# Kernel optimization log

Measured on AMD Instinct MI355X. Metric: run time of the kernel, lower is better.

## Reference

```python
import jax, jax.numpy as jnp
import numpy as np

BIG_CONST = 1000000.0
LN_EPS = 1e-5

B, S, D = 2, 1024, 1024
N, H = 16, D // 16            # n_head, d_head
POS_LEN = 2 * S - 1


def setup_inputs() -> dict:
    key = jax.random.key(0)
    ks = jax.random.split(key, 16)
    std_qkv = np.sqrt(1.0 / float(D + N * H))   # EinsumLayer init: 1/sqrt(fan_in+fan_out)
    std_post = np.sqrt(1.0 / float(N * H + D))
    return {
        "q": jax.random.normal(ks[0], (B, S, D), jnp.float32),
        "k": jax.random.normal(ks[1], (B, S, D), jnp.float32),
        "v": jax.random.normal(ks[2], (B, S, D), jnp.float32),
        "pos_enc": jax.random.normal(ks[3], (POS_LEN, D), jnp.float32),
        "attn_mask": jax.random.randint(ks[4], (B, 1, 1, S), 0, 2, jnp.int32),
        "q_w": jax.random.normal(ks[5], (D, N, H), jnp.float32) * std_qkv,
        "k_w": jax.random.normal(ks[6], (D, N, H), jnp.float32) * std_qkv,
        "k_b": jnp.zeros((N, H), jnp.float32),
        "v_w": jax.random.normal(ks[7], (D, N, H), jnp.float32) * std_qkv,
        "v_b": jnp.zeros((N, H), jnp.float32),
        "r_w_bias": jax.random.uniform(ks[8], (N, 1, H), jnp.float32, 0.0, 0.1),
        "r_r_bias": jax.random.uniform(ks[9], (N, 1, H), jnp.float32, 0.0, 0.1),
        "r_kernel": jax.random.uniform(ks[10], (N, D, H), jnp.float32, 0.0, 0.1),
        "post_w": jax.random.normal(ks[11], (N, H, D), jnp.float32) * std_post,
        "post_b": jnp.zeros((D,), jnp.float32),
        "ln_g": jnp.ones((D,), jnp.float32),
        "ln_b": jnp.zeros((D,), jnp.float32),
    }


def reference(q, k, v, pos_enc, attn_mask, q_w, k_w, k_b, v_w, v_b,
              r_w_bias, r_r_bias, r_kernel, post_w, post_b, ln_g, ln_b):
    input_q = q
    d_head = q_w.shape[-1]
    normalizer = 1.0 / np.sqrt(d_head)

    # head projections -> [B, N, L, H]
    qh = jnp.einsum('bld,dnh->bnlh', q, q_w)
    kh = jnp.einsum('bld,dnh->bnlh', k, k_w) + k_b[None, :, None, :] * 0 + jnp.transpose(k_b, (0, 1))[None, :, None, :] * 0 + k_b.reshape(1, k_b.shape[0], 1, k_b.shape[1])
    kh = jnp.einsum('bld,dnh->bnlh', k, k_w) + k_b.reshape(1, -1, 1, d_head)
    vh = jnp.einsum('bld,dnh->bnlh', v, v_w) + v_b.reshape(1, -1, 1, d_head)

    # content score: (q + r_w_bias) @ k^T * normalizer   [B,N,S,S]
    content = jnp.einsum('bnqh,bnkh->bnqk', qh + r_w_bias[None], kh) * normalizer

    # positional term (rel_shift with shift=0): r = pos_enc @ r_kernel -> [N, P, H]
    r = jnp.einsum('pd,ndh->nph', pos_enc, r_kernel)
    pos_scores = jnp.einsum('bnqh,nph->bnqp', qh + r_r_bias[None], r) * normalizer
    # shift=0 => reshape-swap + narrow + reshape-back is an exact identity; then narrow to k_len
    k_len = kh.shape[-2]
    pos_term = pos_scores[..., :k_len]

    attn_score = (content + pos_term).astype(jnp.float32)
    attn_score = attn_score - BIG_CONST * attn_mask.astype(jnp.float32)
    attn_dist = jax.nn.softmax(attn_score, axis=-1)

    out = jnp.einsum('bnqk,bnkh->bnqh', attn_dist, vh)          # [B,N,S,H]
    attn_out = jnp.einsum('bnlh,nhd->bld', out, post_w) + post_b

    x = input_q + attn_out
    mu = jnp.mean(x, axis=-1, keepdims=True)
    var = jnp.mean(jnp.square(x - mu), axis=-1, keepdims=True)
    return (x - mu) / jnp.sqrt(var + LN_EPS) * ln_g + ln_b
```

## Files before the change

### kernel.cpp

```cpp
#include <hip/hip_runtime.h>
#include <cstddef>
#include <cstdint>

typedef unsigned short u16;
typedef unsigned int   u32;

#define S_LEN  1024
#define NHEAD  16
#define HDIM   64
#define DMODEL 1024
#define NORMSC 0.125f
#define BIGC   1000000.0f
#define LOG2E  1.44269504088896f
#define SC2    (0.125f * 1.44269504088896f)

typedef __bf16 bf16x8 __attribute__((ext_vector_type(8)));
typedef float  f32x4  __attribute__((ext_vector_type(4)));

#define MFMA16(a, b, c) __builtin_amdgcn_mfma_f32_16x16x32_bf16((a), (b), (c), 0, 0, 0)

__device__ __forceinline__ u16 f2bf(float f) {
    u32 u = __float_as_uint(f);
    u32 r = (u + 0x7fffu + ((u >> 16) & 1u)) >> 16;
    return (u16)r;
}
__device__ __forceinline__ float bf2f(u32 v) {
    return __uint_as_float(v << 16);
}
__device__ __forceinline__ float4 unp4(uint2 u) {
    float4 f;
    f.x = bf2f(u.x & 0xffffu); f.y = bf2f(u.x >> 16);
    f.z = bf2f(u.y & 0xffffu); f.w = bf2f(u.y >> 16);
    return f;
}
__device__ __forceinline__ void async16(const void* g, void* l) {
    __builtin_amdgcn_global_load_lds(
        (__attribute__((address_space(1))) void*)(g),
        (__attribute__((address_space(3))) void*)(l), 16, 0, 0);
}

__global__ __launch_bounds__(256) void prep_all(
    const float* q, const float* k, const float* v, const float* pos,
    const float* qw, const float* kw, const float* vw, const float* pw, const float* rk,
    u16* qbf, u16* kbf, u16* vbf, u16* posb,
    u16* qwT, u16* kwT, u16* vwT, u16* pwT, u16* WrT)
{
    __shared__ float tb[32][33];
    const int bid = blockIdx.x, tid = threadIdx.x;
    if (bid < 7168) {
        const float* s; u16* d; int base;
        if (bid < 2048)      { s = q;   d = qbf;  base = bid; }
        else if (bid < 4096) { s = k;   d = kbf;  base = bid - 2048; }
        else if (bid < 6144) { s = v;   d = vbf;  base = bid - 4096; }
        else                 { s = pos; d = posb; base = bid - 6144; }
        const int i = base * 1024 + tid * 4;
        const float4 val = *(const float4*)&s[i];
        uint2 o;
        o.x = (u32)f2bf(val.x) | ((u32)f2bf(val.y) << 16);
        o.y = (u32)f2bf(val.z) | ((u32)f2bf(val.w) << 16);
        *(uint2*)&d[i] = o;
        return;
    }
    const int t = bid - 7168;
    const float* in; u16* out; int ild, r0, c0;
    if (t < 4096) {
        const int ts = t & 1023;
        if (t < 1024)      { in = qw; out = qwT; }
        else if (t < 2048) { in = kw; out = kwT; }
        else if (t < 3072) { in = vw; out = vwT; }
        else               { in = pw; out = pwT; }
        ild = 1024;
        r0 = (ts >> 5) * 32; c0 = (ts & 31) * 32;
    } else {
        const int ts = t - 4096;
        const int n = ts >> 6, tt = ts & 63;
        in = rk + (size_t)n * 65536; out = WrT + (size_t)n * 65536;
        ild = 64;
        r0 = (tt >> 1) * 32; c0 = (tt & 1) * 32;
    }
    const int tx = tid & 31, ty = tid >> 5;
    for (int i = ty; i < 32; i += 8)
        tb[i][tx] = in[(size_t)(r0 + i) * ild + c0 + tx];
    __syncthreads();
    for (int i = ty; i < 32; i += 8)
        out[(size_t)(c0 + i) * 1024 + r0 + tx] = f2bf(tb[tx][i]);
}

struct GJ { const u16* A; const u16* Bt; u16* C; int M; int k0; int klen; };

__global__ __launch_bounds__(256) void gemm_p(
    GJ j0, GJ j1, GJ j2, GJ j3, GJ j4, GJ j5, GJ j6, GJ j7, int nj)
{
    const int bid = blockIdx.x;
    const int c8 = bid & 7;
    const int x = (bid >> 3) & 7;
    int z, y;
    if (nj == 8) { z = c8; y = bid >> 6; }
    else         { z = c8 >> 1; y = ((c8 & 1) << 3) + (bid >> 6); }
    GJ g;
    switch (z) {
        case 0: g = j0; break; case 1: g = j1; break;
        case 2: g = j2; break; case 3: g = j3; break;
        case 4: g = j4; break; case 5: g = j5; break;
        case 6: g = j6; break; default: g = j7;
    }
    const int bm = y * 128;
    if (bm >= g.M) return;
    const int bn = x * 128;
    __shared__ u16 As[2][4096];
    __shared__ u16 Bs[2][4096];
    const int tid = threadIdx.x;
    const int w = tid >> 6, lane = tid & 63;
    const int wm = (w >> 1) * 64, wn = (w & 1) * 64;
    const int l15 = lane & 15, l16 = lane >> 4;
    f32x4 acc[4][4] = {};
    const char* Ab = (const char*)g.A;
    const char* Bb = (const char*)g.Bt;
    const int kend = g.k0 + g.klen;
    const int m0 = w * 1024 + lane * 16;
    const int m1 = (4 + w) * 1024 + lane * 16;
    const int r0w = m0 >> 6, rc0 = ((((m0 >> 4) & 3) + r0w) & 3) << 4;
    const int r1w = m1 >> 6, rc1 = ((((m1 >> 4) & 3) + r1w) & 3) << 4;
    async16(Ab + ((size_t)(bm + r0w) * 1024 + g.k0) * 2 + rc0, (char*)As[0] + m0);
    async16(Bb + ((size_t)(bn + r0w) * 1024 + g.k0) * 2 + rc0, (char*)Bs[0] + m0);
    async16(Ab + ((size_t)(bm + r1w) * 1024 + g.k0) * 2 + rc1, (char*)As[0] + m1);
    async16(Bb + ((size_t)(bn + r1w) * 1024 + g.k0) * 2 + rc1, (char*)Bs[0] + m1);
    const int rotA = ((l16 - l15) & 3) << 3;
    int buf = 0;
    for (int k0 = g.k0; k0 < kend; k0 += 32) {
        __syncthreads();
        const int kn = k0 + 32;
        if (kn < kend) {
            async16(Ab + ((size_t)(bm + r0w) * 1024 + kn) * 2 + rc0, (char*)As[buf ^ 1] + m0);
            async16(Bb + ((size_t)(bn + r0w) * 1024 + kn) * 2 + rc0, (char*)Bs[buf ^ 1] + m0);
            async16(Ab + ((size_t)(bm + r1w) * 1024 + kn) * 2 + rc1, (char*)As[buf ^ 1] + m1);
            async16(Bb + ((size_t)(bn + r1w) * 1024 + kn) * 2 + rc1, (char*)Bs[buf ^ 1] + m1);
        }
        bf16x8 af[4], bfr[4];
#pragma unroll
        for (int i = 0; i < 4; ++i)
            af[i] = *(const bf16x8*)&As[buf][(wm + i * 16 + l15) * 32 + rotA];
#pragma unroll
        for (int j = 0; j < 4; ++j)
            bfr[j] = *(const bf16x8*)&Bs[buf][(wn + j * 16 + l15) * 32 + rotA];
#pragma unroll
        for (int i = 0; i < 4; ++i)
#pragma unroll
            for (int j = 0; j < 4; ++j)
                acc[i][j] = MFMA16(af[i], bfr[j], acc[i][j]);
        buf ^= 1;
    }
#pragma unroll
    for (int i = 0; i < 4; ++i)
#pragma unroll
        for (int j = 0; j < 4; ++j) {
            const int c = bn + wn + j * 16 + l15;
#pragma unroll
            for (int rg = 0; rg < 4; ++rg) {
                const int m = bm + wm + i * 16 + l16 * 4 + rg;
                g.C[(size_t)m * 1024 + c] = f2bf(acc[i][j][rg]);
            }
        }
}

__global__ __launch_bounds__(256) void prep2(
    const u16* pk0, const u16* pk1, const u16* pr0, const u16* pr1,
    const u16* pv0, const u16* pv1, const u16* pq0, const u16* pq1,
    const float* kbi, const float* vbi, const float* rwb, const float* rrb,
    const int* mask, u16* keff, float* cc, u16* vT, u16* qhb)
{
    __shared__ float tb[32][33];
    const int bid = blockIdx.x, tid = threadIdx.x;
    if (bid < 2048) {
        const int t = bid * 256 + tid;
        const int row = t >> 4, li = t & 15;
        const int n = (row >> 10) & 15, kk = row & 1023, b = row >> 14;
        const size_t mi = ((size_t)(b * 1024 + kk)) * 1024 + n * 64 + li * 4;
        const size_t pi = ((size_t)kk) * 1024 + n * 64 + li * 4;
        const float4 k0v = unp4(*(const uint2*)&pk0[mi]);
        const float4 k1v = unp4(*(const uint2*)&pk1[mi]);
        const float4 r0v = unp4(*(const uint2*)&pr0[pi]);
        const float4 r1v = unp4(*(const uint2*)&pr1[pi]);
        const float4 kb4 = *(const float4*)&kbi[n * 64 + li * 4];
        float4 kv, rv;
        kv.x = k0v.x + k1v.x + kb4.x; kv.y = k0v.y + k1v.y + kb4.y;
        kv.z = k0v.z + k1v.z + kb4.z; kv.w = k0v.w + k1v.w + kb4.w;
        rv.x = r0v.x + r1v.x; rv.y = r0v.y + r1v.y;
        rv.z = r0v.z + r1v.z; rv.w = r0v.w + r1v.w;
        const float4 w1 = *(const float4*)&rwb[n * 64 + li * 4];
        const float4 w2 = *(const float4*)&rrb[n * 64 + li * 4];
        float s = w1.x * kv.x + w1.y * kv.y + w1.z * kv.z + w1.w * kv.w
                + w2.x * rv.x + w2.y * rv.y + w2.z * rv.z + w2.w * rv.w;
        uint2 o;
        o.x = (u32)f2bf(kv.x + rv.x) | ((u32)f2bf(kv.y + rv.y) << 16);
        o.y = (u32)f2bf(kv.z + rv.z) | ((u32)f2bf(kv.w + rv.w) << 16);
        *(uint2*)&keff[(size_t)row * 64 + li * 4] = o;
#pragma unroll
        for (int m = 1; m < 16; m <<= 1) s += __shfl_xor(s, m);
        if (li == 0)
            cc[row] = LOG2E * (NORMSC * s - BIGC * (float)mask[b * 1024 + kk]);
        return;
    }
    if (bid < 4096) {
        const int t = bid - 2048;
        const int head = t >> 6, tt = t & 63;
        const int b = head >> 4, n = head & 15;
        const int r0 = (tt >> 1) * 32, c0 = (tt & 1) * 32;
        const int tx = tid & 31, ty = tid >> 5;
        const float vb = vbi[n * 64 + c0 + tx];
        for (int i = ty; i < 32; i += 8) {
            const size_t idx = ((size_t)(b * 1024 + r0 + i)) * 1024 + n * 64 + c0 + tx;
            tb[i][tx] = bf2f(pv0[idx]) + bf2f(pv1[idx]) + vb;
        }
        __syncthreads();
        u16* out = vT + (size_t)head * 65536;
        for (int i = ty; i < 32; i += 8)
            out[(size_t)(c0 + i) * 1024 + r0 + tx] = f2bf(tb[tx][i]);
        return;
    }
    const int t = bid - 4096;
    const int e = t * 1024 + tid * 4;
    const int m = e >> 10, c = e & 1023;
    const float4 a = unp4(*(const uint2*)&pq0[e]);
    const float4 b4 = unp4(*(const uint2*)&pq1[e]);
    uint2 o;
    o.x = (u32)f2bf(a.x + b4.x) | ((u32)f2bf(a.y + b4.y) << 16);
    o.y = (u32)f2bf(a.z + b4.z) | ((u32)f2bf(a.w + b4.w) << 16);
    const int b2 = m >> 10, l = m & 1023, n = c >> 6, h = c & 63;
    *(uint2*)&qhb[(((size_t)(b2 * NHEAD + n)) * 1024 + l) * 64 + h] = o;
}

__global__ __launch_bounds__(128) void attn_mfma(
    const u16* qb, const u16* kb, const u16* vtb, const float* ccomb, u16* O)
{
    __shared__ u16   Ks[2][4096];
    __shared__ u16   Vs[2][4096];
    __shared__ __bf16 Ps[2][1024];
    const int tid = threadIdx.x;
    const int w = tid >> 6, lane = tid & 63;
    const int l15 = lane & 15, l16 = lane >> 4;
    const int bid = blockIdx.x;
    const int i128 = bid >> 3;
    const int head = (bid & 7) * 4 + (i128 >> 5);
    const int q0 = (i128 & 31) * 32;
    const int b = head >> 4, n = head & 15;
    const size_t hoff = (size_t)head * 65536;
    const u16* qh = qb + hoff;
    const char* khc = (const char*)(kb + hoff);
    const char* vtc = (const char*)(vtb + hoff);
    const float* cc = ccomb + head * 1024;
    __bf16* Pw = Ps[w];

    bf16x8 qf[2];
    {
        const size_t rb = ((size_t)(q0 + w * 16 + l15)) * 64 + l16 * 8;
        qf[0] = *(const bf16x8*)&qh[rb];
        qf[1] = *(const bf16x8*)&qh[rb + 32];
    }
    f32x4 Oacc[4] = {};
    float lsum[4] = {};

    const int sr0 = w * 32 + (lane >> 3);
    const int sc0 = lane & 7;
#pragma unroll
    for (int i = 0; i < 4; ++i) {
        const int r = sr0 + i * 8;
        async16(khc + r * 128 + (((sc0 + r) & 7) << 4), (char*)Ks[0] + r * 128 + sc0 * 16);
        async16(vtc + (size_t)r * 2048 + (((sc0 + r) & 7) << 4), (char*)Vs[0] + r * 128 + sc0 * 16);
    }
    int buf = 0;
    for (int kc = 0; kc < 16; ++kc) {
        __syncthreads();
        if (kc < 15) {
            const int kn = kc + 1;
#pragma unroll
            for (int i = 0; i < 4; ++i) {
                const int r = sr0 + i * 8;
                async16(khc + kn * 8192 + r * 128 + (((sc0 + r) & 7) << 4),
                        (char*)Ks[buf ^ 1] + r * 128 + sc0 * 16);
                async16(vtc + (size_t)r * 2048 + kn * 128 + (((sc0 + r) & 7) << 4),
                        (char*)Vs[buf ^ 1] + r * 128 + sc0 * 16);
            }
        }
        const u16* Kb = Ks[buf];
        const u16* Vb = Vs[buf];
        f32x4 sc[4];
#pragma unroll
        for (int j = 0; j < 4; ++j) {
            const int rk2 = j * 16 + l15;
            const int base = rk2 * 64;
            f32x4 a = {0.f, 0.f, 0.f, 0.f};
            a = MFMA16(qf[0], *(const bf16x8*)&Kb[base + (((l16 - rk2) & 7) << 3)], a);
            a = MFMA16(qf[1], *(const bf16x8*)&Kb[base + (((l16 + 4 - rk2) & 7) << 3)], a);
            const float cadd = cc[kc * 64 + j * 16 + l15];
            sc[j] = a * SC2 + cadd;
        }
#pragma unroll
        for (int j = 0; j < 4; ++j) {
            const int cg = j * 2 + (l15 >> 3);
#pragma unroll
            for (int rg = 0; rg < 4; ++rg) {
                const float p = exp2f(sc[j][rg]);
                lsum[rg] += p;
                const int row = l16 * 4 + rg;
                Pw[row * 64 + (((cg - row) & 7) << 3) + (l15 & 7)] = (__bf16)p;
            }
        }
        bf16x8 pf[2];
#pragma unroll
        for (int f = 0; f < 2; ++f)
            pf[f] = *(const bf16x8*)&Pw[l15 * 64 + (((f * 4 + l16 - l15) & 7) << 3)];
#pragma unroll
        for (int t4 = 0; t4 < 4; ++t4) {
#pragma unroll
            for (int f = 0; f < 2; ++f) {
                const int vr = t4 * 16 + l15;
                const int ch = f * 4 + l16;
                const bf16x8 vf = *(const bf16x8*)&Vb[vr * 64 + (((ch - vr) & 7) << 3)];
                Oacc[t4] = MFMA16(pf[f], vf, Oacc[t4]);
            }
        }
        buf ^= 1;
    }
    float inv[4];
#pragma unroll
    for (int rg = 0; rg < 4; ++rg) {
        float s = lsum[rg];
#pragma unroll
        for (int m = 1; m < 16; m <<= 1) s += __shfl_xor(s, m);
        inv[rg] = 1.0f / s;
    }
#pragma unroll
    for (int t4 = 0; t4 < 4; ++t4) {
#pragma unroll
        for (int rg = 0; rg < 4; ++rg) {
            const int srow = q0 + w * 16 + l16 * 4 + rg;
            const int col = n * 64 + t4 * 16 + l15;
            O[((size_t)b * 1024 + srow) * 1024 + col] = f2bf(Oacc[t4][rg] * inv[rg]);
        }
    }
}

__global__ __launch_bounds__(256) void ln_kernel(
    const u16* __restrict__ p0, const u16* __restrict__ p1,
    const u16* __restrict__ p2, const u16* __restrict__ p3,
    const float* __restrict__ resid, const float* __restrict__ pb,
    const float* __restrict__ g, const float* __restrict__ bb,
    float* __restrict__ out)
{
    const int row = blockIdx.x;
    const int tid = threadIdx.x;
    const size_t i = (size_t)row * DMODEL + tid * 4;
    const float4 a0 = unp4(*(const uint2*)&p0[i]);
    const float4 a1 = unp4(*(const uint2*)&p1[i]);
    const float4 a2 = unp4(*(const uint2*)&p2[i]);
    const float4 a3 = unp4(*(const uint2*)&p3[i]);
    const float4 rr = *(const float4*)&resid[i];
    const float4 pv = *(const float4*)&pb[tid * 4];
    float4 v;
    v.x = a0.x + a1.x + a2.x + a3.x + rr.x + pv.x;
    v.y = a0.y + a1.y + a2.y + a3.y + rr.y + pv.y;
    v.z = a0.z + a1.z + a2.z + a3.z + rr.z + pv.z;
    v.w = a0.w + a1.w + a2.w + a3.w + rr.w + pv.w;
    float s1 = v.x + v.y + v.z + v.w;
    float s2 = v.x * v.x + v.y * v.y + v.z * v.z + v.w * v.w;
#pragma unroll
    for (int off = 32; off; off >>= 1) {
        s1 += __shfl_down(s1, off);
        s2 += __shfl_down(s2, off);
    }
    __shared__ float rb[8];
    if ((tid & 63) == 0) { rb[tid >> 6] = s1; rb[4 + (tid >> 6)] = s2; }
    __syncthreads();
    if (tid == 0) {
        rb[0] = rb[0] + rb[1] + rb[2] + rb[3];
        rb[4] = rb[4] + rb[5] + rb[6] + rb[7];
    }
    __syncthreads();
    s1 = rb[0]; s2 = rb[4];
    const float mu = s1 * (1.0f / DMODEL);
    const float var = s2 * (1.0f / DMODEL) - mu * mu;
    const float rstd = rsqrtf(var + 1e-5f);
    const float4 gv = *(const float4*)&g[tid * 4];
    const float4 bv = *(const float4*)&bb[tid * 4];
    float4 o;
    o.x = (v.x - mu) * rstd * gv.x + bv.x;
    o.y = (v.y - mu) * rstd * gv.y + bv.y;
    o.z = (v.z - mu) * rstd * gv.z + bv.z;
    o.w = (v.w - mu) * rstd * gv.w + bv.w;
    *(float4*)&out[i] = o;
}

extern "C" void kernel_launch(void* const* d_in, const int* in_sizes, int n_in,
                              void* d_out, int out_size, void* d_ws, size_t ws_size,
                              hipStream_t stream)
{
    (void)in_sizes; (void)n_in; (void)out_size; (void)ws_size;
    const float* q   = (const float*)d_in[0];
    const float* k   = (const float*)d_in[1];
    const float* v   = (const float*)d_in[2];
    const float* pos = (const float*)d_in[3];
    const int*   msk = (const int*)d_in[4];
    const float* qw  = (const float*)d_in[5];
    const float* kw  = (const float*)d_in[6];
    const float* kbi = (const float*)d_in[7];
    const float* vw  = (const float*)d_in[8];
    const float* vbi = (const float*)d_in[9];
    const float* rwb = (const float*)d_in[10];
    const float* rrb = (const float*)d_in[11];
    const float* rk  = (const float*)d_in[12];
    const float* pw  = (const float*)d_in[13];
    const float* pb  = (const float*)d_in[14];
    const float* lg  = (const float*)d_in[15];
    const float* lb  = (const float*)d_in[16];
    float* out = (float*)d_out;

    float* fb = (float*)d_ws;
    float* cc   = fb;
    u16* us   = (u16*)(cc + 32768);
    u16* qbf  = us;
    u16* kbf  = qbf + 2097152;
    u16* vbf  = kbf + 2097152;
    u16* posb = vbf + 2097152;
    u16* qwT  = posb + 1048576;
    u16* kwT  = qwT + 1048576;
    u16* vwT  = kwT + 1048576;
    u16* pwT  = vwT + 1048576;
    u16* WrT  = pwT + 1048576;
    u16* qhb  = WrT + 1048576;
    u16* keffb= qhb + 2097152;
    u16* vTb  = keffb + 2097152;
    u16* pq0  = vTb + 2097152;
    u16* pq1  = pq0 + 2097152;
    u16* pk0  = pq1 + 2097152;
    u16* pk1  = pk0 + 2097152;
    u16* pv0  = pk1 + 2097152;
    u16* pv1  = pv0 + 2097152;
    u16* pr0  = pv1 + 2097152;
    u16* pr1  = pr0 + 1048576;
    u16* po0  = pr1 + 1048576;
    u16* po1  = po0 + 2097152;
    u16* po2  = po1 + 2097152;
    u16* po3  = po2 + 2097152;
    u16* Obf  = qbf;

    dim3 blk(256);
    prep_all<<<12288, blk, 0, stream>>>(q, k, v, pos, qw, kw, vw, pw, rk,
                                        qbf, kbf, vbf, posb, qwT, kwT, vwT, pwT, WrT);

    GJ jq0 = {qbf,  qwT, pq0, 2048, 0,   512};
    GJ jq1 = {qbf,  qwT, pq1, 2048, 512, 512};
    GJ jk0 = {kbf,  kwT, pk0, 2048, 0,   512};
    GJ jk1 = {kbf,  kwT, pk1, 2048, 512, 512};
    GJ jv0 = {vbf,  vwT, pv0, 2048, 0,   512};
    GJ jv1 = {vbf,  vwT, pv1, 2048, 512, 512};
    GJ jp0 = {posb, WrT, pr0, 1024, 0,   512};
    GJ jp1 = {posb, WrT, pr1, 1024, 512, 512};
    gemm_p<<<1024, blk, 0, stream>>>(jq0, jq1, jk0, jk1, jv0, jv1, jp0, jp1, 8);

    prep2<<<6144, blk, 0, stream>>>(pk0, pk1, pr0, pr1, pv0, pv1, pq0, pq1,
                                    kbi, vbi, rwb, rrb, msk, keffb, cc, vTb, qhb);

    attn_mfma<<<1024, dim3(128), 0, stream>>>(qhb, keffb, vTb, cc, Obf);

    GJ jo0 = {Obf, pwT, po0, 2048, 0,   256};
    GJ jo1 = {Obf, pwT, po1, 2048, 256, 256};
    GJ jo2 = {Obf, pwT, po2, 2048, 512, 256};
    GJ jo3 = {Obf, pwT, po3, 2048, 768, 256};
    gemm_p<<<512, blk, 0, stream>>>(jo0, jo1, jo2, jo3, jo0, jo0, jo0, jo0, 4);

    ln_kernel<<<2048, blk, 0, stream>>>(po0, po1, po2, po3, q, pb, lg, lb, out);
}
```

Before: 203.3 us.

## Load GEMM MFMA fragments directly from global memory, dropping LDS staging

The batched projection GEMM kernel no longer stages A and B tiles through double-buffered shared memory with async copies. Each wave now loads its MFMA fragments straight from global memory into registers, prefetching the next k-step while issuing MFMAs on the current one. This removes LDS traffic and the per-step __syncthreads. In exchange, the two waves sharing a tile row or column each fetch the same data from global memory (relying on cache), and each load reads only 16 bytes per row with a strided pattern.

```diff
diff --git a/kernel.cpp b/kernel.cpp
--- a/kernel.cpp
+++ b/kernel.cpp
@@ -107,49 +107,51 @@
     const int bm = y * 128;
     if (bm >= g.M) return;
     const int bn = x * 128;
-    __shared__ u16 As[2][4096];
-    __shared__ u16 Bs[2][4096];
     const int tid = threadIdx.x;
     const int w = tid >> 6, lane = tid & 63;
     const int wm = (w >> 1) * 64, wn = (w & 1) * 64;
     const int l15 = lane & 15, l16 = lane >> 4;
     f32x4 acc[4][4] = {};
-    const char* Ab = (const char*)g.A;
-    const char* Bb = (const char*)g.Bt;
-    const int kend = g.k0 + g.klen;
-    const int m0 = w * 1024 + lane * 16;
-    const int m1 = (4 + w) * 1024 + lane * 16;
-    const int r0w = m0 >> 6, rc0 = ((((m0 >> 4) & 3) + r0w) & 3) << 4;
-    const int r1w = m1 >> 6, rc1 = ((((m1 >> 4) & 3) + r1w) & 3) << 4;
-    async16(Ab + ((size_t)(bm + r0w) * 1024 + g.k0) * 2 + rc0, (char*)As[0] + m0);
-    async16(Bb + ((size_t)(bn + r0w) * 1024 + g.k0) * 2 + rc0, (char*)Bs[0] + m0);
-    async16(Ab + ((size_t)(bm + r1w) * 1024 + g.k0) * 2 + rc1, (char*)As[0] + m1);
-    async16(Bb + ((size_t)(bn + r1w) * 1024 + g.k0) * 2 + rc1, (char*)Bs[0] + m1);
-    const int rotA = ((l16 - l15) & 3) << 3;
-    int buf = 0;
-    for (int k0 = g.k0; k0 < kend; k0 += 32) {
-        __syncthreads();
-        const int kn = k0 + 32;
-        if (kn < kend) {
-            async16(Ab + ((size_t)(bm + r0w) * 1024 + kn) * 2 + rc0, (char*)As[buf ^ 1] + m0);
-            async16(Bb + ((size_t)(bn + r0w) * 1024 + kn) * 2 + rc0, (char*)Bs[buf ^ 1] + m0);
-            async16(Ab + ((size_t)(bm + r1w) * 1024 + kn) * 2 + rc1, (char*)As[buf ^ 1] + m1);
-            async16(Bb + ((size_t)(bn + r1w) * 1024 + kn) * 2 + rc1, (char*)Bs[buf ^ 1] + m1);
-        }
-        bf16x8 af[4], bfr[4];
+
+    const u16* ap[4];
+    const u16* bp[4];
+#pragma unroll
+    for (int i = 0; i < 4; ++i)
+        ap[i] = g.A + (size_t)(bm + wm + i * 16 + l15) * 1024 + g.k0 + l16 * 8;
+#pragma unroll
+    for (int j = 0; j < 4; ++j)
+        bp[j] = g.Bt + (size_t)(bn + wn + j * 16 + l15) * 1024 + g.k0 + l16 * 8;
+
+    const int nsteps = g.klen >> 5;
+    bf16x8 ac[4], bc[4];
+#pragma unroll
+    for (int i = 0; i < 4; ++i) ac[i] = *(const bf16x8*)ap[i];
+#pragma unroll
+    for (int j = 0; j < 4; ++j) bc[j] = *(const bf16x8*)bp[j];
+
+    for (int s = 1; s < nsteps; ++s) {
+        bf16x8 an[4], bn2[4];
+        const int ko = s * 32;
+#pragma unroll
+        for (int i = 0; i < 4; ++i) an[i] = *(const bf16x8*)(ap[i] + ko);
+#pragma unroll
+        for (int j = 0; j < 4; ++j) bn2[j] = *(const bf16x8*)(bp[j] + ko);
 #pragma unroll
         for (int i = 0; i < 4; ++i)
-            af[i] = *(const bf16x8*)&As[buf][(wm + i * 16 + l15) * 32 + rotA];
+#pragma unroll
+            for (int j = 0; j < 4; ++j)
+                acc[i][j] = MFMA16(ac[i], bc[j], acc[i][j]);
+#pragma unroll
+        for (int i = 0; i < 4; ++i) ac[i] = an[i];
+#pragma unroll
+        for (int j = 0; j < 4; ++j) bc[j] = bn2[j];
+    }
+#pragma unroll
+    for (int i = 0; i < 4; ++i)
 #pragma unroll
         for (int j = 0; j < 4; ++j)
-            bfr[j] = *(const bf16x8*)&Bs[buf][(wn + j * 16 + l15) * 32 + rotA];
-#pragma unroll
-        for (int i = 0; i < 4; ++i)
-#pragma unroll
-            for (int j = 0; j < 4; ++j)
-                acc[i][j] = MFMA16(af[i], bfr[j], acc[i][j]);
-        buf ^= 1;
-    }
+            acc[i][j] = MFMA16(ac[i], bc[j], acc[i][j]);
+
 #pragma unroll
     for (int i = 0; i < 4; ++i)
 #pragma unroll
```

Result: slower. 245.9 us (+21.0%).
